# Kernel optimization log

Hardware: AMD Instinct MI355X
Metric: run time of the kernel (lower is better)

The kernel has to match this reference:

```python
import jax, jax.numpy as jnp
import numpy as np
from jax import lax

IMG_SIZE = 1024.0  # nominal image dimension for generating plausible coords
IOU_THRESHOLD = 0.5


def box_iou(a, b):
    # a: (N,4), b: (M,4) in (x1,y1,x2,y2); returns (N,M) IoU
    area_a = (a[:, 2] - a[:, 0]) * (a[:, 3] - a[:, 1])
    area_b = (b[:, 2] - b[:, 0]) * (b[:, 3] - b[:, 1])
    lt = jnp.maximum(a[:, None, :2], b[None, :, :2])
    rb = jnp.minimum(a[:, None, 2:], b[None, :, 2:])
    wh = jnp.clip(rb - lt, 0.0)
    inter = wh[..., 0] * wh[..., 1]
    return inter / (area_a[:, None] + area_b[None, :] - inter)


def apply_deltas_to_locations(deltas, locations, stride):
    # Faithful to fcos_apply_deltas_to_locations: clip deltas at 0,
    # un-normalize by stride, subtract/add around the center location.
    d = jnp.clip(deltas, 0.0)  # (N,4) = (l, t, r, b)
    xc, yc = locations[:, 0], locations[:, 1]
    x1 = xc - stride * d[:, 0]
    y1 = yc - stride * d[:, 1]
    x2 = xc + stride * d[:, 2]
    y2 = yc + stride * d[:, 3]
    return jnp.stack([x1, y1, x2, y2], axis=1)


def nms_keep(boxes, scores, iou_threshold):
    # Greedy NMS, equivalent to the sequential reference loop:
    # process boxes in decreasing score order; a box survives if it is not
    # suppressed (IoU > thr) by any earlier surviving box.
    n = boxes.shape[0]
    order = jnp.argsort(-scores)  # descending score order
    b = boxes[order]
    iou = box_iou(b, b)  # (N,N), memory-bound pairwise compare
    idx = jnp.arange(n)

    def body(i, keep):
        suppress = (iou[i] > iou_threshold) & (idx > i) & keep[i]
        return keep & ~suppress

    keep_sorted = lax.fori_loop(0, n, body, jnp.ones((n,), dtype=bool))
    # scatter keep mask back to original ordering
    keep_orig = jnp.zeros((n,), dtype=bool).at[order].set(keep_sorted)
    return keep_orig, order, keep_sorted


def setup_inputs() -> dict:
    key = jax.random.key(0)
    k1, k2, k3, k4 = jax.random.split(key, 4)
    N = 8192
    deltas = jax.random.uniform(k1, (N, 4), dtype=jnp.float32) * 8.0  # stride-normalized LTRB
    locations = jax.random.uniform(k2, (N, 2), dtype=jnp.float32) * IMG_SIZE
    scores = jax.random.uniform(k3, (N,), dtype=jnp.float32)
    class_ids = jax.random.randint(k4, (N,), 0, 80, dtype=jnp.int32)
    return {"deltas": deltas, "locations": locations, "scores": scores,
            "class_ids": class_ids, "stride": 8}


def reference(deltas, locations, scores, class_ids, stride):
    # 1) LTRB delta decode (fcos_apply_deltas_to_locations)
    boxes = apply_deltas_to_locations(deltas, locations, stride)
    # 2) class-specific NMS (class_spec_nms): offset boxes per class so that
    #    boxes of different classes never overlap, then run plain NMS.
    max_coordinate = boxes.max()
    offsets = class_ids.astype(boxes.dtype) * (max_coordinate + 1.0)
    boxes_for_nms = boxes + offsets[:, None]
    keep_orig, order, keep_sorted = nms_keep(boxes_for_nms, scores, IOU_THRESHOLD)
    # boxes: decoded boxes; keep_orig: NMS survival mask (original order);
    # order: score-descending permutation (kept indices = order[keep_sorted])
    return boxes, keep_orig, order
```

## Files before the change

### kernel.cpp

```cpp
#include <hip/hip_runtime.h>

typedef unsigned long long u64;
typedef unsigned int u32;

#define NBOX 8192
#define NW64 128
#define NCLASS 80
#define NCMAX 256
#define CHKCAP 256
#define NS 32
#define SLICE 256
#define NBLK 32
#define K1GRID (NS * NBLK + 1)
#define K2GRID (NBLK + NCLASS + 1)

__device__ __forceinline__ u32 f32_mono(float f) {
  u32 u = __float_as_uint(f);
  return (u & 0x80000000u) ? ~u : (u | 0x80000000u);
}
__device__ __forceinline__ float mono_f32(u32 u) {
  u32 b = (u & 0x80000000u) ? (u ^ 0x80000000u) : ~u;
  return __uint_as_float(b);
}
__device__ __forceinline__ u64 readlane64(u64 v, int l) {
  u32 lo = __builtin_amdgcn_readlane((u32)v, l);
  u32 hi = __builtin_amdgcn_readlane((u32)(v >> 32), l);
  return ((u64)hi << 32) | (u64)lo;
}
__device__ __forceinline__ u32 reduce_bmax(const u32* __restrict__ bmax, int t) {
  u32 bm = bmax[t & 31];
#pragma unroll
  for (int off = 16; off > 0; off >>= 1) {
    u32 o = __shfl_xor(bm, off);
    bm = (bm > o) ? bm : o;
  }
  return bm;
}


__global__ __launch_bounds__(256) void rank_decode_kernel(
    const float* __restrict__ scores, const int* __restrict__ class_ids,
    const float4* __restrict__ deltas, const float2* __restrict__ locs,
    const int* __restrict__ stride_p, float4* __restrict__ boxes_out,
    u32* __restrict__ bmax, int* __restrict__ flag, int* __restrict__ rankp) {
  const int t = threadIdx.x;
  const int b = blockIdx.x;

  if (b == NS * NBLK) {
    __shared__ float4 bxA[CHKCAP], bxB[CHKCAP];
    __shared__ int clsA[CHKCAP], clsB[CHKCAP];
    __shared__ int hist[NCLASS];
    __shared__ int na, nb, hitf;
    __shared__ u32 mred[4];
    if (t == 0) { na = 0; nb = 0; hitf = 0; }
    if (t < NCLASS) hist[t] = 0;
    float s = (float)(*stride_p);
    u32 mymax = 0;
    for (int base = 0; base < NBOX; base += 256) {
      int i = base + t;
      float4 d = deltas[i];
      d.x = fmaxf(d.x, 0.f); d.y = fmaxf(d.y, 0.f);
      d.z = fmaxf(d.z, 0.f); d.w = fmaxf(d.w, 0.f);
      float2 c = locs[i];
      float x1 = c.x - s * d.x, y1 = c.y - s * d.y;
      float x2 = c.x + s * d.z, y2 = c.y + s * d.w;
      float m = fmaxf(fmaxf(x1, y1), fmaxf(x2, y2));
      u32 u = f32_mono(m);
      mymax = mymax > u ? mymax : u;
    }
#pragma unroll
    for (int off = 32; off > 0; off >>= 1) {
      u32 o = __shfl_xor(mymax, off);
      mymax = mymax > o ? mymax : o;
    }
    if ((t & 63) == 0) mred[t >> 6] = mymax;
    __syncthreads();
    u32 g0 = mred[0] > mred[1] ? mred[0] : mred[1];
    u32 g1 = mred[2] > mred[3] ? mred[2] : mred[3];
    float M = mono_f32(g0 > g1 ? g0 : g1);
    float thrA = M - 65.0f;
    for (int base = 0; base < NBOX; base += 256) {
      int i = base + t;
      float4 d = deltas[i];
      d.x = fmaxf(d.x, 0.f); d.y = fmaxf(d.y, 0.f);
      d.z = fmaxf(d.z, 0.f); d.w = fmaxf(d.w, 0.f);
      float2 c = locs[i];
      float4 bb;
      bb.x = c.x - s * d.x; bb.y = c.y - s * d.y;
      bb.z = c.x + s * d.z; bb.w = c.y + s * d.w;
      int cls = class_ids[i];
      atomicAdd(&hist[cls], 1);
      if (bb.z > thrA && bb.w > thrA) {
        int p = atomicAdd(&na, 1);
        if (p < CHKCAP) { bxA[p] = bb; clsA[p] = cls; }
      }
      if (bb.x < 1.0f && bb.y < 1.0f) {
        int p = atomicAdd(&nb, 1);
        if (p < CHKCAP) { bxB[p] = bb; clsB[p] = cls; }
      }
    }
    __syncthreads();
    if (t < NCLASS && hist[t] > NCMAX) atomicOr(&hitf, 1);
    int NA = na < CHKCAP ? na : CHKCAP;
    int NB = nb < CHKCAP ? nb : CHKCAP;
    bool hit = (t == 0) && (na > CHKCAP || nb > CHKCAP);
    for (int pr = t; pr < NA * NB; pr += 256) {
      int a = pr / NB, b2 = pr % NB;
      if (clsB[b2] != clsA[a] + 1) continue;
      float offa = (float)clsA[a] * (M + 1.0f);
      float offb = (float)clsB[b2] * (M + 1.0f);
      float4 A = bxA[a], Bb = bxB[b2];
      A.x += offa; A.y += offa; A.z += offa; A.w += offa;
      Bb.x += offb; Bb.y += offb; Bb.z += offb; Bb.w += offb;
      float ltx = fmaxf(A.x, Bb.x), lty = fmaxf(A.y, Bb.y);
      float rbx = fminf(A.z, Bb.z), rby = fminf(A.w, Bb.w);
      float ww = fmaxf(rbx - ltx, 0.f), hh = fmaxf(rby - lty, 0.f);
      float inter = ww * hh;
      float aa = (A.z - A.x) * (A.w - A.y);
      float ab = (Bb.z - Bb.x) * (Bb.w - Bb.y);
      float iou = inter / (aa + ab - inter);
      if (iou > 0.4f) hit = true;
    }
    if (hit) atomicOr(&hitf, 1);
    __syncthreads();
    if (t == 0) *flag = hitf;
    return;
  }

  const int bi = b & 31;
  const int slice = b >> 5;
  const int i = bi * 256 + t;

  __shared__ u32 st[SLICE];
  __shared__ u32 wmax[4];

  if (slice == 0) {
    float s = (float)(*stride_p);
    float4 d = deltas[i];
    d.x = fmaxf(d.x, 0.f); d.y = fmaxf(d.y, 0.f);
    d.z = fmaxf(d.z, 0.f); d.w = fmaxf(d.w, 0.f);
    float2 c = locs[i];
    float4 bb;
    bb.x = c.x - s * d.x;
    bb.y = c.y - s * d.y;
    bb.z = c.x + s * d.z;
    bb.w = c.y + s * d.w;
    boxes_out[i] = bb;
    float m = fmaxf(fmaxf(bb.x, bb.y), fmaxf(bb.z, bb.w));
    u32 u = f32_mono(m);
#pragma unroll
    for (int off = 32; off > 0; off >>= 1) {
      u32 o = __shfl_xor(u, off);
      u = (u > o) ? u : o;
    }
    if ((t & 63) == 0) wmax[t >> 6] = u;
  }

  st[t] = f32_mono(scores[slice * 256 + t]);
  __syncthreads();
  if (slice == 0 && t == 0) {
    u32 m0 = wmax[0] > wmax[1] ? wmax[0] : wmax[1];
    u32 m1 = wmax[2] > wmax[3] ? wmax[2] : wmax[3];
    bmax[bi] = m0 > m1 ? m0 : m1;
  }

  u32 mi = f32_mono(scores[i]);
  int tp = i - slice * 256;
  int cnt = 0;
#pragma unroll 8
  for (int p = 0; p < SLICE; ++p) {
    u32 mj = st[p];
    bool less = (mj > mi) || (mj == mi && p < tp);
    cnt += less ? 1 : 0;
  }
  rankp[slice * NBOX + i] = cnt;
}

__global__ __launch_bounds__(256) void scatter_nms_kernel(
    const float* __restrict__ scores, const int* __restrict__ class_ids,
    const float4* __restrict__ boxes, const u32* __restrict__ bmax,
    const int* __restrict__ rankp, u64* __restrict__ keys,
    float4* __restrict__ bnms, float* __restrict__ order_out,
    float* __restrict__ keep_out, const int* __restrict__ flag) {
  const int t = threadIdx.x;
  const int bid = blockIdx.x;

  __shared__ u64 ck[NCMAX];
  __shared__ u32 slist[NCMAX];
  __shared__ float4 bx[NCMAX];
  __shared__ u64 smask[NCMAX][4];
  __shared__ int cnt_s;
  __shared__ u32 perm[NBOX];
  __shared__ u64 remv[NW64];

  if (bid < NBLK) {
    int i = bid * 256 + t;
    int r = 0;
#pragma unroll
    for (int s2 = 0; s2 < NS; ++s2) r += rankp[s2 * NBOX + i];
    float maxc = mono_f32(reduce_bmax(bmax, t));
    u32 mi = f32_mono(scores[i]);
    keys[r] = ((u64)(~mi) << 32) | (u32)i;
    int cls = class_ids[i];
    float off = (float)cls * (maxc + 1.0f);
    float4 bb = boxes[i];
    bb.x += off; bb.y += off; bb.z += off; bb.w += off;
    bnms[r] = bb;
    order_out[r] = (float)i;
    return;
  }

  if (bid < NBLK + NCLASS) {
    const int c = bid - NBLK;
    if (*flag != 0) return;
    if (t == 0) cnt_s = 0;
    __syncthreads();

    {
      int nxtc = class_ids[t];
      float nxts = scores[t];
      for (int base = 0; base < NBOX; base += 256) {
        int cur = nxtc;
        float cs = nxts;
        if (base + 256 < NBOX) {
          nxtc = class_ids[base + 256 + t];
          nxts = scores[base + 256 + t];
        }
        if (cur == c) {
          int p = atomicAdd(&cnt_s, 1);
          if (p < NCMAX) ck[p] = ((u64)(~f32_mono(cs)) << 32) | (u32)(base + t);
        }
      }
    }
    __syncthreads();
    int nc = cnt_s;
    if (nc > NCMAX) return;
    if (t < nc) {
      u64 kme = ck[t];
      int r2 = 0;
      for (int p = 0; p < nc; ++p) r2 += (ck[p] < kme) ? 1 : 0;
      slist[r2] = (u32)kme;
    }
    __syncthreads();

    float maxc = mono_f32(reduce_bmax(bmax, t));
    float off = (float)c * (maxc + 1.0f);
    for (int k = t; k < nc; k += 256) {
      float4 bb = boxes[slist[k]];
      bb.x += off; bb.y += off; bb.z += off; bb.w += off;
      bx[k] = bb;
    }
    __syncthreads();

    {
      const int wv = t >> 6;
      const int lane = t & 63;
      const int nw = (nc + 63) >> 6;
      for (int i = wv; i < nc; i += 4) {
        float4 bi = bx[i];
        float area_i = (bi.z - bi.x) * (bi.w - bi.y);
        for (int w = 0; w < nw; ++w) {
          int j2 = w * 64 + lane;
          float4 bj = bx[j2 < NCMAX ? j2 : 0];
          float ltx = fmaxf(bi.x, bj.x), lty = fmaxf(bi.y, bj.y);
          float rbx = fminf(bi.z, bj.z), rby = fminf(bi.w, bj.w);
          float ww = fmaxf(rbx - ltx, 0.f), hh = fmaxf(rby - lty, 0.f);
          float inter = ww * hh;
          float area_j = (bj.z - bj.x) * (bj.w - bj.y);
          float iou = inter / (area_i + area_j - inter);
          bool p = (iou > 0.5f) && (j2 > i) && (j2 < nc);
          u64 mm = __ballot(p);
          if (lane == 0) smask[i][w] = mm;
        }
      }
    }
    __syncthreads();
    if (t >= 64) return;

    u64 ma[4], mb[4], mc[4], md[4];
#pragma unroll
    for (int w = 0; w < 4; ++w) {
      ma[w] = smask[t][w];
      mb[w] = smask[64 + t][w];
      mc[w] = smask[128 + t][w];
      md[w] = smask[192 + t][w];
    }
    u64 R0 = 0, R1 = 0, R2 = 0, R3 = 0;
    u64 K0 = 0, K1 = 0, K2 = 0, K3 = 0;

#define SCAND(D, MD, RD, KD)                                                   \
  {                                                                            \
    int lim = nc - (D) * 64;                                                   \
    if (lim > 0) {                                                             \
      if (lim > 64) lim = 64;                                                  \
      for (int ii = 0; ii < lim; ++ii) {                                       \
        u64 kb = ((RD >> ii) & 1ull) ^ 1ull;                                   \
        KD |= kb << ii;                                                        \
        u64 sm2 = 0ull - kb;                                                   \
        R0 |= readlane64(MD[0], ii) & sm2;                                     \
        R1 |= readlane64(MD[1], ii) & sm2;                                     \
        R2 |= readlane64(MD[2], ii) & sm2;                                     \
        R3 |= readlane64(MD[3], ii) & sm2;                                     \
      }                                                                        \
    }                                                                          \
  }
    SCAND(0, ma, R0, K0)
    SCAND(1, mb, R1, K1)
    SCAND(2, mc, R2, K2)
    SCAND(3, md, R3, K3)
#undef SCAND

    u64 kk[4] = {K0, K1, K2, K3};
#pragma unroll
    for (int d = 0; d < 4; ++d) {
      int j = d * 64 + t;
      if (j < nc) keep_out[slist[j]] = ((kk[d] >> t) & 1ull) ? 1.0f : 0.0f;
    }
    return;
  }

  if (*flag == 0) return;
  for (int k = t; k < NW64; k += 256) remv[k] = 0;
  for (int i = t; i < NBOX; i += 256) {
    int r = 0;
#pragma unroll
    for (int s2 = 0; s2 < NS; ++s2) r += rankp[s2 * NBOX + i];
    perm[r] = (u32)i;
  }
  __syncthreads();
  float maxc = mono_f32(reduce_bmax(bmax, t));
  if (t < 64) {
    int lane = t;
    for (int ii = 0; ii < NBOX; ++ii) {
      if ((remv[ii >> 6] >> (ii & 63)) & 1ull) continue;
      u32 pi = perm[ii];
      float offi = (float)class_ids[pi] * (maxc + 1.0f);
      float4 bi = boxes[pi];
      bi.x += offi; bi.y += offi; bi.z += offi; bi.w += offi;
      float area_i = (bi.z - bi.x) * (bi.w - bi.y);
      for (int jb = ii + 1; jb < NBOX; jb += 64) {
        int j = jb + lane;
        bool p = false;
        if (j < NBOX) {
          u32 pj = perm[j];
          float offj = (float)class_ids[pj] * (maxc + 1.0f);
          float4 bj = boxes[pj];
          bj.x += offj; bj.y += offj; bj.z += offj; bj.w += offj;
          float ltx = fmaxf(bi.x, bj.x), lty = fmaxf(bi.y, bj.y);
          float rbx = fminf(bi.z, bj.z), rby = fminf(bi.w, bj.w);
          float ww = fmaxf(rbx - ltx, 0.f), hh = fmaxf(rby - lty, 0.f);
          float inter = ww * hh;
          float area_j = (bj.z - bj.x) * (bj.w - bj.y);
          float iou = inter / (area_i + area_j - inter);
          p = iou > 0.5f;
        }
        u64 m = __ballot(p);
        if (lane == 0 && m) {
          int w0 = jb >> 6, sh = jb & 63;
          remv[w0] |= (m << sh);
          if (sh && (w0 + 1) < NW64) remv[w0 + 1] |= (m >> (64 - sh));
        }
      }
    }
  }
  __syncthreads();
  for (int k = t; k < NBOX; k += 256)
    keep_out[perm[k]] = ((remv[k >> 6] >> (k & 63)) & 1ull) ? 0.0f : 1.0f;
}

extern "C" void kernel_launch(void* const* d_in, const int* in_sizes, int n_in,
                              void* d_out, int out_size, void* d_ws, size_t ws_size,
                              hipStream_t stream) {
  const float* deltas = (const float*)d_in[0];
  const float* locs = (const float*)d_in[1];
  const float* scores = (const float*)d_in[2];
  const int* class_ids = (const int*)d_in[3];
  const int* stride_p = (const int*)d_in[4];

  float* boxes_out = (float*)d_out;
  float* keep_out = (float*)d_out + (size_t)NBOX * 4;
  float* order_out = (float*)d_out + (size_t)NBOX * 5;

  u32* bmax = (u32*)((char*)d_ws + 64);
  int* flag = (int*)((char*)d_ws + 256);
  u64* keys = (u64*)((char*)d_ws + 4096);
  float4* bnms = (float4*)((char*)d_ws + 4096 + 65536);
  int* rankp = (int*)((char*)d_ws + 4096 + 65536 + 131072);

  rank_decode_kernel<<<K1GRID, 256, 0, stream>>>(
      scores, class_ids, (const float4*)deltas, (const float2*)locs, stride_p,
      (float4*)boxes_out, bmax, flag, rankp);

  scatter_nms_kernel<<<K2GRID, 256, 0, stream>>>(
      scores, class_ids, (const float4*)boxes_out, bmax, rankp, keys, bnms,
      order_out, keep_out, flag);
}
```

Measured before the change: 51.97 us.

## Move per-class NMS into first kernel, recomputing boxes and max locally

```diff
diff --git a/kernel.cpp b/kernel.cpp
--- a/kernel.cpp
+++ b/kernel.cpp
@@ -11,8 +11,9 @@
 #define NS 32
 #define SLICE 256
 #define NBLK 32
-#define K1GRID (NS * NBLK + 1)
-#define K2GRID (NBLK + NCLASS + 1)
+#define RANKB (NS * NBLK)
+#define K1GRID (RANKB + 1 + NCLASS)
+#define K2GRID (NBLK + 1)
 
 __device__ __forceinline__ u32 f32_mono(float f) {
   u32 u = __float_as_uint(f);
@@ -38,15 +39,67 @@
 }
 
 
-__global__ __launch_bounds__(256) void rank_decode_kernel(
+__global__ __launch_bounds__(256) void fused_kernel(
     const float* __restrict__ scores, const int* __restrict__ class_ids,
     const float4* __restrict__ deltas, const float2* __restrict__ locs,
     const int* __restrict__ stride_p, float4* __restrict__ boxes_out,
-    u32* __restrict__ bmax, int* __restrict__ flag, int* __restrict__ rankp) {
+    float* __restrict__ keep_out, u32* __restrict__ bmax,
+    int* __restrict__ flag, int* __restrict__ rankp) {
   const int t = threadIdx.x;
   const int b = blockIdx.x;
 
-  if (b == NS * NBLK) {
+  if (b < RANKB) {
+    const int bi = b & 31;
+    const int slice = b >> 5;
+    const int i = bi * 256 + t;
+
+    __shared__ u32 st[SLICE];
+    __shared__ u32 wmax[4];
+
+    if (slice == 0) {
+      float s = (float)(*stride_p);
+      float4 d = deltas[i];
+      d.x = fmaxf(d.x, 0.f); d.y = fmaxf(d.y, 0.f);
+      d.z = fmaxf(d.z, 0.f); d.w = fmaxf(d.w, 0.f);
+      float2 c = locs[i];
+      float4 bb;
+      bb.x = c.x - s * d.x;
+      bb.y = c.y - s * d.y;
+      bb.z = c.x + s * d.z;
+      bb.w = c.y + s * d.w;
+      boxes_out[i] = bb;
+      float m = fmaxf(fmaxf(bb.x, bb.y), fmaxf(bb.z, bb.w));
+      u32 u = f32_mono(m);
+#pragma unroll
+      for (int off = 32; off > 0; off >>= 1) {
+        u32 o = __shfl_xor(u, off);
+        u = (u > o) ? u : o;
+      }
+      if ((t & 63) == 0) wmax[t >> 6] = u;
+    }
+
+    st[t] = f32_mono(scores[slice * 256 + t]);
+    __syncthreads();
+    if (slice == 0 && t == 0) {
+      u32 m0 = wmax[0] > wmax[1] ? wmax[0] : wmax[1];
+      u32 m1 = wmax[2] > wmax[3] ? wmax[2] : wmax[3];
+      bmax[bi] = m0 > m1 ? m0 : m1;
+    }
+
+    u32 mi = f32_mono(scores[i]);
+    int tp = i - slice * 256;
+    int cnt = 0;
+#pragma unroll 8
+    for (int p = 0; p < SLICE; ++p) {
+      u32 mj = st[p];
+      bool less = (mj > mi) || (mj == mi && p < tp);
+      cnt += less ? 1 : 0;
+    }
+    rankp[slice * NBOX + i] = cnt;
+    return;
+  }
+
+  if (b == RANKB) {
     __shared__ float4 bxA[CHKCAP], bxB[CHKCAP];
     __shared__ int clsA[CHKCAP], clsB[CHKCAP];
     __shared__ int hist[NCLASS];
@@ -127,166 +180,119 @@
     return;
   }
 
-  const int bi = b & 31;
-  const int slice = b >> 5;
-  const int i = bi * 256 + t;
-
-  __shared__ u32 st[SLICE];
-  __shared__ u32 wmax[4];
-
-  if (slice == 0) {
-    float s = (float)(*stride_p);
-    float4 d = deltas[i];
-    d.x = fmaxf(d.x, 0.f); d.y = fmaxf(d.y, 0.f);
-    d.z = fmaxf(d.z, 0.f); d.w = fmaxf(d.w, 0.f);
-    float2 c = locs[i];
-    float4 bb;
-    bb.x = c.x - s * d.x;
-    bb.y = c.y - s * d.y;
-    bb.z = c.x + s * d.z;
-    bb.w = c.y + s * d.w;
-    boxes_out[i] = bb;
-    float m = fmaxf(fmaxf(bb.x, bb.y), fmaxf(bb.z, bb.w));
-    u32 u = f32_mono(m);
-#pragma unroll
-    for (int off = 32; off > 0; off >>= 1) {
-      u32 o = __shfl_xor(u, off);
-      u = (u > o) ? u : o;
-    }
-    if ((t & 63) == 0) wmax[t >> 6] = u;
-  }
-
-  st[t] = f32_mono(scores[slice * 256 + t]);
-  __syncthreads();
-  if (slice == 0 && t == 0) {
-    u32 m0 = wmax[0] > wmax[1] ? wmax[0] : wmax[1];
-    u32 m1 = wmax[2] > wmax[3] ? wmax[2] : wmax[3];
-    bmax[bi] = m0 > m1 ? m0 : m1;
-  }
-
-  u32 mi = f32_mono(scores[i]);
-  int tp = i - slice * 256;
-  int cnt = 0;
-#pragma unroll 8
-  for (int p = 0; p < SLICE; ++p) {
-    u32 mj = st[p];
-    bool less = (mj > mi) || (mj == mi && p < tp);
-    cnt += less ? 1 : 0;
-  }
-  rankp[slice * NBOX + i] = cnt;
-}
-
-__global__ __launch_bounds__(256) void scatter_nms_kernel(
-    const float* __restrict__ scores, const int* __restrict__ class_ids,
-    const float4* __restrict__ boxes, const u32* __restrict__ bmax,
-    const int* __restrict__ rankp, u64* __restrict__ keys,
-    float4* __restrict__ bnms, float* __restrict__ order_out,
-    float* __restrict__ keep_out, const int* __restrict__ flag) {
-  const int t = threadIdx.x;
-  const int bid = blockIdx.x;
-
+  const int c = b - (RANKB + 1);
   __shared__ u64 ck[NCMAX];
   __shared__ u32 slist[NCMAX];
   __shared__ float4 bx[NCMAX];
   __shared__ u64 smask[NCMAX][4];
+  __shared__ u32 cmred[4];
   __shared__ int cnt_s;
-  __shared__ u32 perm[NBOX];
-  __shared__ u64 remv[NW64];
-
-  if (bid < NBLK) {
-    int i = bid * 256 + t;
-    int r = 0;
-#pragma unroll
-    for (int s2 = 0; s2 < NS; ++s2) r += rankp[s2 * NBOX + i];
-    float maxc = mono_f32(reduce_bmax(bmax, t));
-    u32 mi = f32_mono(scores[i]);
-    keys[r] = ((u64)(~mi) << 32) | (u32)i;
-    int cls = class_ids[i];
-    float off = (float)cls * (maxc + 1.0f);
-    float4 bb = boxes[i];
-    bb.x += off; bb.y += off; bb.z += off; bb.w += off;
-    bnms[r] = bb;
-    order_out[r] = (float)i;
-    return;
-  }
-
-  if (bid < NBLK + NCLASS) {
-    const int c = bid - NBLK;
-    if (*flag != 0) return;
-    if (t == 0) cnt_s = 0;
-    __syncthreads();
-
-    {
-      int nxtc = class_ids[t];
-      float nxts = scores[t];
-      for (int base = 0; base < NBOX; base += 256) {
-        int cur = nxtc;
-        float cs = nxts;
-        if (base + 256 < NBOX) {
-          nxtc = class_ids[base + 256 + t];
-          nxts = scores[base + 256 + t];
-        }
-        if (cur == c) {
-          int p = atomicAdd(&cnt_s, 1);
-          if (p < NCMAX) ck[p] = ((u64)(~f32_mono(cs)) << 32) | (u32)(base + t);
-        }
-      }
-    }
-    __syncthreads();
-    int nc = cnt_s;
-    if (nc > NCMAX) return;
-    if (t < nc) {
-      u64 kme = ck[t];
-      int r2 = 0;
-      for (int p = 0; p < nc; ++p) r2 += (ck[p] < kme) ? 1 : 0;
-      slist[r2] = (u32)kme;
-    }
-    __syncthreads();
-
-    float maxc = mono_f32(reduce_bmax(bmax, t));
-    float off = (float)c * (maxc + 1.0f);
-    for (int k = t; k < nc; k += 256) {
-      float4 bb = boxes[slist[k]];
-      bb.x += off; bb.y += off; bb.z += off; bb.w += off;
-      bx[k] = bb;
-    }
-    __syncthreads();
-
-    {
-      const int wv = t >> 6;
-      const int lane = t & 63;
-      const int nw = (nc + 63) >> 6;
-      for (int i = wv; i < nc; i += 4) {
-        float4 bi = bx[i];
-        float area_i = (bi.z - bi.x) * (bi.w - bi.y);
-        for (int w = 0; w < nw; ++w) {
-          int j2 = w * 64 + lane;
-          float4 bj = bx[j2 < NCMAX ? j2 : 0];
-          float ltx = fmaxf(bi.x, bj.x), lty = fmaxf(bi.y, bj.y);
-          float rbx = fminf(bi.z, bj.z), rby = fminf(bi.w, bj.w);
-          float ww = fmaxf(rbx - ltx, 0.f), hh = fmaxf(rby - lty, 0.f);
-          float inter = ww * hh;
-          float area_j = (bj.z - bj.x) * (bj.w - bj.y);
-          float iou = inter / (area_i + area_j - inter);
-          bool p = (iou > 0.5f) && (j2 > i) && (j2 < nc);
-          u64 mm = __ballot(p);
-          if (lane == 0) smask[i][w] = mm;
-        }
-      }
-    }
-    __syncthreads();
-    if (t >= 64) return;
-
-    u64 ma[4], mb[4], mc[4], md[4];
-#pragma unroll
-    for (int w = 0; w < 4; ++w) {
-      ma[w] = smask[t][w];
-      mb[w] = smask[64 + t][w];
-      mc[w] = smask[128 + t][w];
-      md[w] = smask[192 + t][w];
-    }
-    u64 R0 = 0, R1 = 0, R2 = 0, R3 = 0;
-    u64 K0 = 0, K1 = 0, K2 = 0, K3 = 0;
+  if (t == 0) cnt_s = 0;
+
+  float s = (float)(*stride_p);
+  u32 mymax = 0;
+  for (int base = 0; base < NBOX; base += 256) {
+    int i = base + t;
+    float4 d = deltas[i];
+    d.x = fmaxf(d.x, 0.f); d.y = fmaxf(d.y, 0.f);
+    d.z = fmaxf(d.z, 0.f); d.w = fmaxf(d.w, 0.f);
+    float2 cc = locs[i];
+    float x1 = cc.x - s * d.x, y1 = cc.y - s * d.y;
+    float x2 = cc.x + s * d.z, y2 = cc.y + s * d.w;
+    float m = fmaxf(fmaxf(x1, y1), fmaxf(x2, y2));
+    u32 u = f32_mono(m);
+    mymax = mymax > u ? mymax : u;
+  }
+#pragma unroll
+  for (int off = 32; off > 0; off >>= 1) {
+    u32 o = __shfl_xor(mymax, off);
+    mymax = mymax > o ? mymax : o;
+  }
+  if ((t & 63) == 0) cmred[t >> 6] = mymax;
+  __syncthreads();
+  u32 g0 = cmred[0] > cmred[1] ? cmred[0] : cmred[1];
+  u32 g1 = cmred[2] > cmred[3] ? cmred[2] : cmred[3];
+  float M = mono_f32(g0 > g1 ? g0 : g1);
+  float off = (float)c * (M + 1.0f);
+
+  {
+    int nxtc = class_ids[t];
+    float nxts = scores[t];
+    for (int base = 0; base < NBOX; base += 256) {
+      int cur = nxtc;
+      float cs = nxts;
+      if (base + 256 < NBOX) {
+        nxtc = class_ids[base + 256 + t];
+        nxts = scores[base + 256 + t];
+      }
+      if (cur == c) {
+        int p = atomicAdd(&cnt_s, 1);
+        if (p < NCMAX) ck[p] = ((u64)(~f32_mono(cs)) << 32) | (u32)(base + t);
+      }
+    }
+  }
+  __syncthreads();
+  int nc = cnt_s;
+  if (nc > NCMAX) return;
+
+  if (t < nc) {
+    u64 kme = ck[t];
+    int r2 = 0;
+    for (int p = 0; p < nc; ++p) r2 += (ck[p] < kme) ? 1 : 0;
+    slist[r2] = (u32)kme;
+  }
+  __syncthreads();
+
+  for (int k = t; k < nc; k += 256) {
+    u32 idx = slist[k];
+    float4 d = deltas[idx];
+    d.x = fmaxf(d.x, 0.f); d.y = fmaxf(d.y, 0.f);
+    d.z = fmaxf(d.z, 0.f); d.w = fmaxf(d.w, 0.f);
+    float2 cc = locs[idx];
+    float4 bb;
+    bb.x = (cc.x - s * d.x) + off;
+    bb.y = (cc.y - s * d.y) + off;
+    bb.z = (cc.x + s * d.z) + off;
+    bb.w = (cc.y + s * d.w) + off;
+    bx[k] = bb;
+  }
+  __syncthreads();
+
+  {
+    const int wv = t >> 6;
+    const int lane = t & 63;
+    const int nw = (nc + 63) >> 6;
+    for (int i = wv; i < nc; i += 4) {
+      float4 bi = bx[i];
+      float area_i = (bi.z - bi.x) * (bi.w - bi.y);
+      for (int w = 0; w < nw; ++w) {
+        int j2 = w * 64 + lane;
+        float4 bj = bx[j2 < NCMAX ? j2 : 0];
+        float ltx = fmaxf(bi.x, bj.x), lty = fmaxf(bi.y, bj.y);
+        float rbx = fminf(bi.z, bj.z), rby = fminf(bi.w, bj.w);
+        float ww = fmaxf(rbx - ltx, 0.f), hh = fmaxf(rby - lty, 0.f);
+        float inter = ww * hh;
+        float area_j = (bj.z - bj.x) * (bj.w - bj.y);
+        float iou = inter / (area_i + area_j - inter);
+        bool p = (iou > 0.5f) && (j2 > i) && (j2 < nc);
+        u64 mm = __ballot(p);
+        if (lane == 0) smask[i][w] = mm;
+      }
+    }
+  }
+  __syncthreads();
+  if (t >= 64) return;
+
+  u64 ma[4], mb[4], mc[4], md[4];
+#pragma unroll
+  for (int w = 0; w < 4; ++w) {
+    ma[w] = smask[t][w];
+    mb[w] = smask[64 + t][w];
+    mc[w] = smask[128 + t][w];
+    md[w] = smask[192 + t][w];
+  }
+  u64 R0 = 0, R1 = 0, R2 = 0, R3 = 0;
+  u64 K0 = 0, K1 = 0, K2 = 0, K3 = 0;
 
 #define SCAND(D, MD, RD, KD)                                                   \
   {                                                                            \
@@ -304,22 +310,40 @@
       }                                                                        \
     }                                                                          \
   }
-    SCAND(0, ma, R0, K0)
-    SCAND(1, mb, R1, K1)
-    SCAND(2, mc, R2, K2)
-    SCAND(3, md, R3, K3)
+  SCAND(0, ma, R0, K0)
+  SCAND(1, mb, R1, K1)
+  SCAND(2, mc, R2, K2)
+  SCAND(3, md, R3, K3)
 #undef SCAND
 
-    u64 kk[4] = {K0, K1, K2, K3};
-#pragma unroll
-    for (int d = 0; d < 4; ++d) {
-      int j = d * 64 + t;
-      if (j < nc) keep_out[slist[j]] = ((kk[d] >> t) & 1ull) ? 1.0f : 0.0f;
-    }
+  u64 kk[4] = {K0, K1, K2, K3};
+#pragma unroll
+  for (int d = 0; d < 4; ++d) {
+    int j = d * 64 + t;
+    if (j < nc) keep_out[slist[j]] = ((kk[d] >> t) & 1ull) ? 1.0f : 0.0f;
+  }
+}
+
+__global__ __launch_bounds__(256) void scatter_fallback_kernel(
+    const int* __restrict__ class_ids, const float4* __restrict__ boxes,
+    const u32* __restrict__ bmax, const int* __restrict__ rankp,
+    float* __restrict__ order_out, float* __restrict__ keep_out,
+    const int* __restrict__ flag) {
+  const int t = threadIdx.x;
+  const int bid = blockIdx.x;
+
+  if (bid < NBLK) {
+    int i = bid * 256 + t;
+    int r = 0;
+#pragma unroll
+    for (int s2 = 0; s2 < NS; ++s2) r += rankp[s2 * NBOX + i];
+    order_out[r] = (float)i;
     return;
   }
 
   if (*flag == 0) return;
+  __shared__ u32 perm[NBOX];
+  __shared__ u64 remv[NW64];
   for (int k = t; k < NW64; k += 256) remv[k] = 0;
   for (int i = t; i < NBOX; i += 256) {
     int r = 0;
@@ -383,15 +407,13 @@
 
   u32* bmax = (u32*)((char*)d_ws + 64);
   int* flag = (int*)((char*)d_ws + 256);
-  u64* keys = (u64*)((char*)d_ws + 4096);
-  float4* bnms = (float4*)((char*)d_ws + 4096 + 65536);
-  int* rankp = (int*)((char*)d_ws + 4096 + 65536 + 131072);
-
-  rank_decode_kernel<<<K1GRID, 256, 0, stream>>>(
+  int* rankp = (int*)((char*)d_ws + 4096);
+
+  fused_kernel<<<K1GRID, 256, 0, stream>>>(
       scores, class_ids, (const float4*)deltas, (const float2*)locs, stride_p,
-      (float4*)boxes_out, bmax, flag, rankp);
-
-  scatter_nms_kernel<<<K2GRID, 256, 0, stream>>>(
-      scores, class_ids, (const float4*)boxes_out, bmax, rankp, keys, bnms,
-      order_out, keep_out, flag);
-}
+      (float4*)boxes_out, keep_out, bmax, flag, rankp);
+
+  scatter_fallback_kernel<<<K2GRID, 256, 0, stream>>>(
+      class_ids, (const float4*)boxes_out, bmax, rankp, order_out, keep_out,
+      flag);
+}
```

Measured after the change: 44.71 us. 1.16x faster.

## Split decode into its own kernel and overlap per-class NMS with ranking

Applied to the files above, without the earlier changes.

```diff
diff --git a/kernel.cpp b/kernel.cpp
--- a/kernel.cpp
+++ b/kernel.cpp
@@ -11,8 +11,9 @@
 #define NS 32
 #define SLICE 256
 #define NBLK 32
-#define K1GRID (NS * NBLK + 1)
-#define K2GRID (NBLK + NCLASS + 1)
+#define RANKB (NS * NBLK)
+#define K2GRID (RANKB + 1 + NCLASS)
+#define K3GRID (NBLK + 1)
 
 __device__ __forceinline__ u32 f32_mono(float f) {
   u32 u = __float_as_uint(f);
@@ -38,56 +39,81 @@
 }
 
 
-__global__ __launch_bounds__(256) void rank_decode_kernel(
-    const float* __restrict__ scores, const int* __restrict__ class_ids,
+__global__ __launch_bounds__(256) void decode_kernel(
     const float4* __restrict__ deltas, const float2* __restrict__ locs,
     const int* __restrict__ stride_p, float4* __restrict__ boxes_out,
-    u32* __restrict__ bmax, int* __restrict__ flag, int* __restrict__ rankp) {
+    u32* __restrict__ bmax) {
+  const int t = threadIdx.x;
+  const int i = blockIdx.x * 256 + t;
+  __shared__ u32 wmax[4];
+  float s = (float)(*stride_p);
+  float4 d = deltas[i];
+  d.x = fmaxf(d.x, 0.f); d.y = fmaxf(d.y, 0.f);
+  d.z = fmaxf(d.z, 0.f); d.w = fmaxf(d.w, 0.f);
+  float2 c = locs[i];
+  float4 bb;
+  bb.x = c.x - s * d.x;
+  bb.y = c.y - s * d.y;
+  bb.z = c.x + s * d.z;
+  bb.w = c.y + s * d.w;
+  boxes_out[i] = bb;
+  float m = fmaxf(fmaxf(bb.x, bb.y), fmaxf(bb.z, bb.w));
+  u32 u = f32_mono(m);
+#pragma unroll
+  for (int off = 32; off > 0; off >>= 1) {
+    u32 o = __shfl_xor(u, off);
+    u = (u > o) ? u : o;
+  }
+  if ((t & 63) == 0) wmax[t >> 6] = u;
+  __syncthreads();
+  if (t == 0) {
+    u32 m0 = wmax[0] > wmax[1] ? wmax[0] : wmax[1];
+    u32 m1 = wmax[2] > wmax[3] ? wmax[2] : wmax[3];
+    bmax[blockIdx.x] = m0 > m1 ? m0 : m1;
+  }
+}
+
+__global__ __launch_bounds__(256) void rank_nms_kernel(
+    const float* __restrict__ scores, const int* __restrict__ class_ids,
+    const float4* __restrict__ boxes, const u32* __restrict__ bmax,
+    float* __restrict__ keep_out, int* __restrict__ flag,
+    int* __restrict__ rankp) {
   const int t = threadIdx.x;
   const int b = blockIdx.x;
 
-  if (b == NS * NBLK) {
+  if (b < RANKB) {
+    const int bi = b & 31;
+    const int slice = b >> 5;
+    const int i = bi * 256 + t;
+    __shared__ u32 st[SLICE];
+    st[t] = f32_mono(scores[slice * 256 + t]);
+    __syncthreads();
+    u32 mi = f32_mono(scores[i]);
+    int tp = i - slice * 256;
+    int cnt = 0;
+#pragma unroll 8
+    for (int p = 0; p < SLICE; ++p) {
+      u32 mj = st[p];
+      bool less = (mj > mi) || (mj == mi && p < tp);
+      cnt += less ? 1 : 0;
+    }
+    rankp[slice * NBOX + i] = cnt;
+    return;
+  }
+
+  if (b == RANKB) {
     __shared__ float4 bxA[CHKCAP], bxB[CHKCAP];
     __shared__ int clsA[CHKCAP], clsB[CHKCAP];
     __shared__ int hist[NCLASS];
     __shared__ int na, nb, hitf;
-    __shared__ u32 mred[4];
     if (t == 0) { na = 0; nb = 0; hitf = 0; }
     if (t < NCLASS) hist[t] = 0;
-    float s = (float)(*stride_p);
-    u32 mymax = 0;
-    for (int base = 0; base < NBOX; base += 256) {
-      int i = base + t;
-      float4 d = deltas[i];
-      d.x = fmaxf(d.x, 0.f); d.y = fmaxf(d.y, 0.f);
-      d.z = fmaxf(d.z, 0.f); d.w = fmaxf(d.w, 0.f);
-      float2 c = locs[i];
-      float x1 = c.x - s * d.x, y1 = c.y - s * d.y;
-      float x2 = c.x + s * d.z, y2 = c.y + s * d.w;
-      float m = fmaxf(fmaxf(x1, y1), fmaxf(x2, y2));
-      u32 u = f32_mono(m);
-      mymax = mymax > u ? mymax : u;
-    }
-#pragma unroll
-    for (int off = 32; off > 0; off >>= 1) {
-      u32 o = __shfl_xor(mymax, off);
-      mymax = mymax > o ? mymax : o;
-    }
-    if ((t & 63) == 0) mred[t >> 6] = mymax;
     __syncthreads();
-    u32 g0 = mred[0] > mred[1] ? mred[0] : mred[1];
-    u32 g1 = mred[2] > mred[3] ? mred[2] : mred[3];
-    float M = mono_f32(g0 > g1 ? g0 : g1);
+    float M = mono_f32(reduce_bmax(bmax, t));
     float thrA = M - 65.0f;
     for (int base = 0; base < NBOX; base += 256) {
       int i = base + t;
-      float4 d = deltas[i];
-      d.x = fmaxf(d.x, 0.f); d.y = fmaxf(d.y, 0.f);
-      d.z = fmaxf(d.z, 0.f); d.w = fmaxf(d.w, 0.f);
-      float2 c = locs[i];
-      float4 bb;
-      bb.x = c.x - s * d.x; bb.y = c.y - s * d.y;
-      bb.z = c.x + s * d.z; bb.w = c.y + s * d.w;
+      float4 bb = boxes[i];
       int cls = class_ids[i];
       atomicAdd(&hist[cls], 1);
       if (bb.z > thrA && bb.w > thrA) {
@@ -127,166 +153,87 @@
     return;
   }
 
-  const int bi = b & 31;
-  const int slice = b >> 5;
-  const int i = bi * 256 + t;
-
-  __shared__ u32 st[SLICE];
-  __shared__ u32 wmax[4];
-
-  if (slice == 0) {
-    float s = (float)(*stride_p);
-    float4 d = deltas[i];
-    d.x = fmaxf(d.x, 0.f); d.y = fmaxf(d.y, 0.f);
-    d.z = fmaxf(d.z, 0.f); d.w = fmaxf(d.w, 0.f);
-    float2 c = locs[i];
-    float4 bb;
-    bb.x = c.x - s * d.x;
-    bb.y = c.y - s * d.y;
-    bb.z = c.x + s * d.z;
-    bb.w = c.y + s * d.w;
-    boxes_out[i] = bb;
-    float m = fmaxf(fmaxf(bb.x, bb.y), fmaxf(bb.z, bb.w));
-    u32 u = f32_mono(m);
-#pragma unroll
-    for (int off = 32; off > 0; off >>= 1) {
-      u32 o = __shfl_xor(u, off);
-      u = (u > o) ? u : o;
-    }
-    if ((t & 63) == 0) wmax[t >> 6] = u;
-  }
-
-  st[t] = f32_mono(scores[slice * 256 + t]);
-  __syncthreads();
-  if (slice == 0 && t == 0) {
-    u32 m0 = wmax[0] > wmax[1] ? wmax[0] : wmax[1];
-    u32 m1 = wmax[2] > wmax[3] ? wmax[2] : wmax[3];
-    bmax[bi] = m0 > m1 ? m0 : m1;
-  }
-
-  u32 mi = f32_mono(scores[i]);
-  int tp = i - slice * 256;
-  int cnt = 0;
-#pragma unroll 8
-  for (int p = 0; p < SLICE; ++p) {
-    u32 mj = st[p];
-    bool less = (mj > mi) || (mj == mi && p < tp);
-    cnt += less ? 1 : 0;
-  }
-  rankp[slice * NBOX + i] = cnt;
-}
-
-__global__ __launch_bounds__(256) void scatter_nms_kernel(
-    const float* __restrict__ scores, const int* __restrict__ class_ids,
-    const float4* __restrict__ boxes, const u32* __restrict__ bmax,
-    const int* __restrict__ rankp, u64* __restrict__ keys,
-    float4* __restrict__ bnms, float* __restrict__ order_out,
-    float* __restrict__ keep_out, const int* __restrict__ flag) {
-  const int t = threadIdx.x;
-  const int bid = blockIdx.x;
-
+  const int c = b - (RANKB + 1);
   __shared__ u64 ck[NCMAX];
   __shared__ u32 slist[NCMAX];
   __shared__ float4 bx[NCMAX];
   __shared__ u64 smask[NCMAX][4];
   __shared__ int cnt_s;
-  __shared__ u32 perm[NBOX];
-  __shared__ u64 remv[NW64];
-
-  if (bid < NBLK) {
-    int i = bid * 256 + t;
-    int r = 0;
-#pragma unroll
-    for (int s2 = 0; s2 < NS; ++s2) r += rankp[s2 * NBOX + i];
-    float maxc = mono_f32(reduce_bmax(bmax, t));
-    u32 mi = f32_mono(scores[i]);
-    keys[r] = ((u64)(~mi) << 32) | (u32)i;
-    int cls = class_ids[i];
-    float off = (float)cls * (maxc + 1.0f);
-    float4 bb = boxes[i];
+  if (t == 0) cnt_s = 0;
+  __syncthreads();
+
+  float M = mono_f32(reduce_bmax(bmax, t));
+  float off = (float)c * (M + 1.0f);
+
+  {
+    const int4* ci4 = (const int4*)class_ids;
+    const float4* sc4 = (const float4*)scores;
+#pragma unroll
+    for (int it = 0; it < 8; ++it) {
+      int g = it * 256 + t;
+      int4 c4 = ci4[g];
+      float4 s4 = sc4[g];
+      int e = g * 4;
+      if (c4.x == c) { int p = atomicAdd(&cnt_s, 1); if (p < NCMAX) ck[p] = ((u64)(~f32_mono(s4.x)) << 32) | (u32)(e); }
+      if (c4.y == c) { int p = atomicAdd(&cnt_s, 1); if (p < NCMAX) ck[p] = ((u64)(~f32_mono(s4.y)) << 32) | (u32)(e + 1); }
+      if (c4.z == c) { int p = atomicAdd(&cnt_s, 1); if (p < NCMAX) ck[p] = ((u64)(~f32_mono(s4.z)) << 32) | (u32)(e + 2); }
+      if (c4.w == c) { int p = atomicAdd(&cnt_s, 1); if (p < NCMAX) ck[p] = ((u64)(~f32_mono(s4.w)) << 32) | (u32)(e + 3); }
+    }
+  }
+  __syncthreads();
+  int nc = cnt_s;
+  if (nc > NCMAX) return;
+
+  if (t < nc) {
+    u64 kme = ck[t];
+    int r2 = 0;
+    for (int p = 0; p < nc; ++p) r2 += (ck[p] < kme) ? 1 : 0;
+    slist[r2] = (u32)kme;
+  }
+  __syncthreads();
+
+  for (int k = t; k < nc; k += 256) {
+    float4 bb = boxes[slist[k]];
     bb.x += off; bb.y += off; bb.z += off; bb.w += off;
-    bnms[r] = bb;
-    order_out[r] = (float)i;
-    return;
-  }
-
-  if (bid < NBLK + NCLASS) {
-    const int c = bid - NBLK;
-    if (*flag != 0) return;
-    if (t == 0) cnt_s = 0;
-    __syncthreads();
-
-    {
-      int nxtc = class_ids[t];
-      float nxts = scores[t];
-      for (int base = 0; base < NBOX; base += 256) {
-        int cur = nxtc;
-        float cs = nxts;
-        if (base + 256 < NBOX) {
-          nxtc = class_ids[base + 256 + t];
-          nxts = scores[base + 256 + t];
-        }
-        if (cur == c) {
-          int p = atomicAdd(&cnt_s, 1);
-          if (p < NCMAX) ck[p] = ((u64)(~f32_mono(cs)) << 32) | (u32)(base + t);
-        }
+    bx[k] = bb;
+  }
+  __syncthreads();
+
+  {
+    const int wv = t >> 6;
+    const int lane = t & 63;
+    const int nw = (nc + 63) >> 6;
+    for (int i = wv; i < nc; i += 4) {
+      float4 bi = bx[i];
+      float area_i = (bi.z - bi.x) * (bi.w - bi.y);
+      for (int w = 0; w < nw; ++w) {
+        int j2 = w * 64 + lane;
+        float4 bj = bx[j2 < NCMAX ? j2 : 0];
+        float ltx = fmaxf(bi.x, bj.x), lty = fmaxf(bi.y, bj.y);
+        float rbx = fminf(bi.z, bj.z), rby = fminf(bi.w, bj.w);
+        float ww = fmaxf(rbx - ltx, 0.f), hh = fmaxf(rby - lty, 0.f);
+        float inter = ww * hh;
+        float area_j = (bj.z - bj.x) * (bj.w - bj.y);
+        float iou = inter / (area_i + area_j - inter);
+        bool p = (iou > 0.5f) && (j2 > i) && (j2 < nc);
+        u64 mm = __ballot(p);
+        if (lane == 0) smask[i][w] = mm;
       }
     }
-    __syncthreads();
-    int nc = cnt_s;
-    if (nc > NCMAX) return;
-    if (t < nc) {
-      u64 kme = ck[t];
-      int r2 = 0;
-      for (int p = 0; p < nc; ++p) r2 += (ck[p] < kme) ? 1 : 0;
-      slist[r2] = (u32)kme;
-    }
-    __syncthreads();
-
-    float maxc = mono_f32(reduce_bmax(bmax, t));
-    float off = (float)c * (maxc + 1.0f);
-    for (int k = t; k < nc; k += 256) {
-      float4 bb = boxes[slist[k]];
-      bb.x += off; bb.y += off; bb.z += off; bb.w += off;
-      bx[k] = bb;
-    }
-    __syncthreads();
-
-    {
-      const int wv = t >> 6;
-      const int lane = t & 63;
-      const int nw = (nc + 63) >> 6;
-      for (int i = wv; i < nc; i += 4) {
-        float4 bi = bx[i];
-        float area_i = (bi.z - bi.x) * (bi.w - bi.y);
-        for (int w = 0; w < nw; ++w) {
-          int j2 = w * 64 + lane;
-          float4 bj = bx[j2 < NCMAX ? j2 : 0];
-          float ltx = fmaxf(bi.x, bj.x), lty = fmaxf(bi.y, bj.y);
-          float rbx = fminf(bi.z, bj.z), rby = fminf(bi.w, bj.w);
-          float ww = fmaxf(rbx - ltx, 0.f), hh = fmaxf(rby - lty, 0.f);
-          float inter = ww * hh;
-          float area_j = (bj.z - bj.x) * (bj.w - bj.y);
-          float iou = inter / (area_i + area_j - inter);
-          bool p = (iou > 0.5f) && (j2 > i) && (j2 < nc);
-          u64 mm = __ballot(p);
-          if (lane == 0) smask[i][w] = mm;
-        }
-      }
-    }
-    __syncthreads();
-    if (t >= 64) return;
-
-    u64 ma[4], mb[4], mc[4], md[4];
-#pragma unroll
-    for (int w = 0; w < 4; ++w) {
-      ma[w] = smask[t][w];
-      mb[w] = smask[64 + t][w];
-      mc[w] = smask[128 + t][w];
-      md[w] = smask[192 + t][w];
-    }
-    u64 R0 = 0, R1 = 0, R2 = 0, R3 = 0;
-    u64 K0 = 0, K1 = 0, K2 = 0, K3 = 0;
+  }
+  __syncthreads();
+  if (t >= 64) return;
+
+  u64 ma[4], mb[4], mc[4], md[4];
+#pragma unroll
+  for (int w = 0; w < 4; ++w) {
+    ma[w] = smask[t][w];
+    mb[w] = smask[64 + t][w];
+    mc[w] = smask[128 + t][w];
+    md[w] = smask[192 + t][w];
+  }
+  u64 R0 = 0, R1 = 0, R2 = 0, R3 = 0;
+  u64 K0 = 0, K1 = 0, K2 = 0, K3 = 0;
 
 #define SCAND(D, MD, RD, KD)                                                   \
   {                                                                            \
@@ -304,22 +251,40 @@
       }                                                                        \
     }                                                                          \
   }
-    SCAND(0, ma, R0, K0)
-    SCAND(1, mb, R1, K1)
-    SCAND(2, mc, R2, K2)
-    SCAND(3, md, R3, K3)
+  SCAND(0, ma, R0, K0)
+  SCAND(1, mb, R1, K1)
+  SCAND(2, mc, R2, K2)
+  SCAND(3, md, R3, K3)
 #undef SCAND
 
-    u64 kk[4] = {K0, K1, K2, K3};
-#pragma unroll
-    for (int d = 0; d < 4; ++d) {
-      int j = d * 64 + t;
-      if (j < nc) keep_out[slist[j]] = ((kk[d] >> t) & 1ull) ? 1.0f : 0.0f;
-    }
+  u64 kk[4] = {K0, K1, K2, K3};
+#pragma unroll
+  for (int d = 0; d < 4; ++d) {
+    int j = d * 64 + t;
+    if (j < nc) keep_out[slist[j]] = ((kk[d] >> t) & 1ull) ? 1.0f : 0.0f;
+  }
+}
+
+__global__ __launch_bounds__(256) void scatter_fallback_kernel(
+    const int* __restrict__ class_ids, const float4* __restrict__ boxes,
+    const u32* __restrict__ bmax, const int* __restrict__ rankp,
+    float* __restrict__ order_out, float* __restrict__ keep_out,
+    const int* __restrict__ flag) {
+  const int t = threadIdx.x;
+  const int bid = blockIdx.x;
+
+  if (bid < NBLK) {
+    int i = bid * 256 + t;
+    int r = 0;
+#pragma unroll
+    for (int s2 = 0; s2 < NS; ++s2) r += rankp[s2 * NBOX + i];
+    order_out[r] = (float)i;
     return;
   }
 
   if (*flag == 0) return;
+  __shared__ u32 perm[NBOX];
+  __shared__ u64 remv[NW64];
   for (int k = t; k < NW64; k += 256) remv[k] = 0;
   for (int i = t; i < NBOX; i += 256) {
     int r = 0;
@@ -383,15 +348,17 @@
 
   u32* bmax = (u32*)((char*)d_ws + 64);
   int* flag = (int*)((char*)d_ws + 256);
-  u64* keys = (u64*)((char*)d_ws + 4096);
-  float4* bnms = (float4*)((char*)d_ws + 4096 + 65536);
-  int* rankp = (int*)((char*)d_ws + 4096 + 65536 + 131072);
-
-  rank_decode_kernel<<<K1GRID, 256, 0, stream>>>(
-      scores, class_ids, (const float4*)deltas, (const float2*)locs, stride_p,
-      (float4*)boxes_out, bmax, flag, rankp);
-
-  scatter_nms_kernel<<<K2GRID, 256, 0, stream>>>(
-      scores, class_ids, (const float4*)boxes_out, bmax, rankp, keys, bnms,
-      order_out, keep_out, flag);
-}
+  int* rankp = (int*)((char*)d_ws + 4096);
+
+  decode_kernel<<<NBLK, 256, 0, stream>>>(
+      (const float4*)deltas, (const float2*)locs, stride_p,
+      (float4*)boxes_out, bmax);
+
+  rank_nms_kernel<<<K2GRID, 256, 0, stream>>>(
+      scores, class_ids, (const float4*)boxes_out, bmax, keep_out, flag,
+      rankp);
+
+  scatter_fallback_kernel<<<K3GRID, 256, 0, stream>>>(
+      class_ids, (const float4*)boxes_out, bmax, rankp, order_out, keep_out,
+      flag);
+}
```

New measurement: 45.64 us. -12.2%, faster.
